# Optimization experiments

Hardware: AMD Instinct MI355X
Metric: run time of the kernel (lower is better)

Reference implementation:

```python
import jax, jax.numpy as jnp
import numpy as np

NEG_SLOPE = 0.01  # torch LeakyReLU default

def setup_inputs() -> dict:
    key = jax.random.key(0)
    ks = jax.random.split(key, 16)
    B, T = 256, 168
    LAG, LAT, WS, H = 168, 128, 64, 1024
    def lin(kw, kb, out_f, in_f):
        bound = 1.0 / np.sqrt(in_f)
        W = jax.random.uniform(kw, (out_f, in_f), jnp.float32, -bound, bound)
        b = jax.random.uniform(kb, (out_f,), jnp.float32, -bound, bound)
        return W, b
    W1, b1 = lin(ks[0], ks[1], 64, LAG)
    W2, b2 = lin(ks[2], ks[3], LAT, 64)
    W3, b3 = lin(ks[4], ks[5], H, LAT)
    bound = 1.0 / np.sqrt(H)
    Wih = jax.random.uniform(ks[6], (3 * H, WS), jnp.float32, -bound, bound)
    Whh = jax.random.uniform(ks[7], (3 * H, H), jnp.float32, -bound, bound)
    bih = jax.random.uniform(ks[8], (3 * H,), jnp.float32, -bound, bound)
    bhh = jax.random.uniform(ks[9], (3 * H,), jnp.float32, -bound, bound)
    Wo, bo = lin(ks[10], ks[11], 1, H)
    lag = jax.random.normal(ks[12], (B, LAG), jnp.float32)
    curr = jax.random.normal(ks[13], (T, B, WS), jnp.float32)
    return dict(lag=lag, curr=curr, W1=W1, b1=b1, W2=W2, b2=b2, W3=W3, b3=b3,
                Wih=Wih, Whh=Whh, bih=bih, bhh=bhh, Wo=Wo, bo=bo)

def _leaky(x):
    return jnp.where(x >= 0, x, NEG_SLOPE * x)

def reference(lag, curr, W1, b1, W2, b2, W3, b3, Wih, Whh, bih, bhh, Wo, bo):
    # Encoder MLP: lag -> 64 -> latent -> hidden (leaky relu after first two)
    h = _leaky(lag @ W1.T + b1)
    h = _leaky(h @ W2.T + b2)
    h0 = h @ W3.T + b3  # [B, H]
    H = h0.shape[-1]

    def step(h_t, x_t):
        gi = x_t @ Wih.T + bih          # [B, 3H]
        gh = h_t @ Whh.T + bhh          # [B, 3H]
        ir, iz, inn = jnp.split(gi, 3, axis=-1)
        hr, hz, hn = jnp.split(gh, 3, axis=-1)
        r = jax.nn.sigmoid(ir + hr)
        z = jax.nn.sigmoid(iz + hz)
        n = jnp.tanh(inn + r * hn)
        h_new = (1.0 - z) * n + z * h_t
        return h_new, h_new

    _, hs = jax.lax.scan(step, h0, curr)          # hs: [T, B, H]
    preds = jnp.squeeze(hs @ Wo.T + bo, -1)       # [T, B]
    return preds.T                                 # [B, T]
```

## Files before the change

### kernel.cpp

```cpp
#include <hip/hip_runtime.h>
#include <hip/hip_bf16.h>
#include <cstdint>
#include <cstddef>

typedef _Float16 half8 __attribute__((ext_vector_type(8)));
typedef _Float16 half4 __attribute__((ext_vector_type(4)));
typedef float floatx4 __attribute__((ext_vector_type(4)));
typedef unsigned long long u64;

#define B_ 256
#define T_ 168
#define H_ 1024
#define WS_ 64
#define LAG_ 168
#define LAT_ 128
#define SENT 0xFFFFFFFFFFFFFFFFull

__device__ __forceinline__ float fast_sigmoid(float x) {
    return __builtin_amdgcn_rcpf(1.f + __expf(-x));
}
__device__ __forceinline__ float fast_tanh(float x) {
    return 1.f - 2.f * __builtin_amdgcn_rcpf(__expf(2.f * x) + 1.f);
}

__global__ void cvt_all(const float4* __restrict__ a, half4* __restrict__ da, int na,
                        const float4* __restrict__ b, half4* __restrict__ db, int nb,
                        const float4* __restrict__ c, half4* __restrict__ dc, int nc) {
    int i = blockIdx.x * blockDim.x + threadIdx.x;
    const float4* s;
    half4* d;
    int j = i;
    if (j < na) { s = a; d = da; }
    else {
        j -= na;
        if (j < nb) { s = b; d = db; }
        else {
            j -= nb;
            if (j >= nc) return;
            s = c; d = dc;
        }
    }
    float4 v = s[j];
    half4 o;
    o[0] = (_Float16)v.x; o[1] = (_Float16)v.y;
    o[2] = (_Float16)v.z; o[3] = (_Float16)v.w;
    d[j] = o;
}

__global__ void enc_fused(const float* __restrict__ lag,
                          const float* __restrict__ W1, const float* __restrict__ b1,
                          const float* __restrict__ W2, const float* __restrict__ b2,
                          const float* __restrict__ W3, const float* __restrict__ b3,
                          float* __restrict__ hprev32, _Float16* __restrict__ h0f16) {
    __shared__ float lrow[LAG_];
    __shared__ float l1[64];
    __shared__ float l2[LAT_];
    const int r = blockIdx.x, tid = threadIdx.x;
    if (tid < LAG_) lrow[tid] = lag[(size_t)r * LAG_ + tid];
    __syncthreads();
    if (tid < 64) {
        const float* w = W1 + (size_t)tid * LAG_;
        float s = b1[tid];
        for (int k = 0; k < LAG_; ++k) s += lrow[k] * w[k];
        l1[tid] = (s >= 0.f) ? s : 0.01f * s;
    }
    __syncthreads();
    if (tid < LAT_) {
        const float* w = W2 + (size_t)tid * 64;
        float s = b2[tid];
        for (int k = 0; k < 64; ++k) s += l1[k] * w[k];
        l2[tid] = (s >= 0.f) ? s : 0.01f * s;
    }
    __syncthreads();
    for (int j = tid; j < H_; j += 256) {
        const float* w = W3 + (size_t)j * LAT_;
        float acc = b3[j];
        #pragma unroll 8
        for (int k = 0; k < LAT_; ++k) acc += l2[k] * w[k];
        hprev32[(size_t)r * H_ + j] = acc;
        h0f16[(size_t)r * H_ + j]   = (_Float16)acc;
    }
}

__global__ __launch_bounds__(256, 1) void gru_sentinel(
    _Float16* __restrict__ hring,
    const float* __restrict__ hprev32, const _Float16* __restrict__ whh16,
    const _Float16* __restrict__ wih16, const _Float16* __restrict__ x16,
    const float* __restrict__ bih, const float* __restrict__ bhh,
    const float* __restrict__ Wo, float* __restrict__ partials)
{
    __shared__ __align__(16) _Float16 Ash[2][16 * 1032];
    __shared__ __align__(16) _Float16 Wsh[192 * 72];
    __shared__ __align__(16) _Float16 Hsh[4 * 256];

    const int tid  = threadIdx.x;
    const int w    = tid >> 6;
    const int lane = tid & 63;
    const int m16  = lane & 15;
    const int quad = lane >> 4;
    const int pi   = blockIdx.x & 15;
    const int qi   = blockIdx.x >> 4;
    const int pi16 = pi << 4;
    const int u    = (qi << 6) + (w << 4) + m16;

    for (int idx = tid; idx < 1536; idx += 256) {
        int rowl = idx >> 3, ch = idx & 7;
        int g = rowl >> 6, ru = rowl & 63;
        *(uint4*)(&Wsh[rowl * 72 + (ch << 3)]) =
            *(const uint4*)(wih16 + (size_t)(((g << 10) + (qi << 6) + ru) << 6) + (ch << 3));
    }

    half8 br[32], bz[32], bn[32];
    {
        const _Float16* p0 = whh16 + ((size_t)u << 10) + (quad << 3);
        const _Float16* p1 = whh16 + ((size_t)(H_ + u) << 10) + (quad << 3);
        const _Float16* p2 = whh16 + ((size_t)(2 * H_ + u) << 10) + (quad << 3);
        #pragma unroll
        for (int c = 0; c < 32; ++c) br[c] = *(const half8*)(p0 + (c << 5));
        #pragma unroll
        for (int c = 0; c < 32; ++c) bz[c] = *(const half8*)(p1 + (c << 5));
        #pragma unroll
        for (int c = 0; c < 32; ++c) bn[c] = *(const half8*)(p2 + (c << 5));
    }

    const float b_r  = bih[u]          + bhh[u];
    const float b_z  = bih[H_ + u]     + bhh[H_ + u];
    const float b_in = bih[2 * H_ + u];
    const float b_hn = bhh[2 * H_ + u];
    const float wo_u = Wo[u];

    float hreg[4];
    #pragma unroll
    for (int i = 0; i < 4; ++i)
        hreg[i] = hprev32[((size_t)(pi16 + (quad << 2) + i) << 10) + u];

    __syncthreads();

    const int srow = tid >> 4;
    const int sch  = tid & 15;
    const int prow = lane >> 2;
    const int pc4  = lane & 3;

    for (int t = 0; t < T_; ++t) {
        const _Float16* hsrc = hring + (size_t)t * (B_ * H_);
        _Float16*       hdst = hring + (size_t)(t + 1) * (B_ * H_);

        half8 ax0 = *(const half8*)(x16 + (((size_t)t << 8) + pi16 + m16) * WS_ + (quad << 3));
        half8 ax1 = *(const half8*)(x16 + (((size_t)t << 8) + pi16 + m16) * WS_ + 32 + (quad << 3));

        u64 va[4][4];
        const _Float16* s = hsrc + ((size_t)(pi16 + srow) << 10) + (sch << 4);
        #pragma unroll
        for (int g = 0; g < 4; ++g)
            #pragma unroll
            for (int k = 0; k < 4; ++k)
                va[g][k] = __hip_atomic_load((const u64*)(s + (g << 8) + (k << 2)),
                                             __ATOMIC_RELAXED, __HIP_MEMORY_SCOPE_AGENT);

        floatx4 acc_r  = {b_r,  b_r,  b_r,  b_r };
        floatx4 acc_z  = {b_z,  b_z,  b_z,  b_z };
        floatx4 acc_in = {b_in, b_in, b_in, b_in};
        floatx4 acc_hn = {b_hn, b_hn, b_hn, b_hn};

        {
            half8 p0 = *(const half8*)(&Wsh[((w << 4) + m16) * 72        + (quad << 3)]);
            half8 p1 = *(const half8*)(&Wsh[(64 + (w << 4) + m16) * 72   + (quad << 3)]);
            half8 p2 = *(const half8*)(&Wsh[(128 + (w << 4) + m16) * 72  + (quad << 3)]);
            acc_r  = __builtin_amdgcn_mfma_f32_16x16x32_f16(ax0, p0, acc_r,  0, 0, 0);
            acc_z  = __builtin_amdgcn_mfma_f32_16x16x32_f16(ax0, p1, acc_z,  0, 0, 0);
            acc_in = __builtin_amdgcn_mfma_f32_16x16x32_f16(ax0, p2, acc_in, 0, 0, 0);
            half8 q0 = *(const half8*)(&Wsh[((w << 4) + m16) * 72        + 32 + (quad << 3)]);
            half8 q1 = *(const half8*)(&Wsh[(64 + (w << 4) + m16) * 72   + 32 + (quad << 3)]);
            half8 q2 = *(const half8*)(&Wsh[(128 + (w << 4) + m16) * 72  + 32 + (quad << 3)]);
            acc_r  = __builtin_amdgcn_mfma_f32_16x16x32_f16(ax1, q0, acc_r,  0, 0, 0);
            acc_z  = __builtin_amdgcn_mfma_f32_16x16x32_f16(ax1, q1, acc_z,  0, 0, 0);
            acc_in = __builtin_amdgcn_mfma_f32_16x16x32_f16(ax1, q2, acc_in, 0, 0, 0);
        }

        for (;;) {
            bool miss = false;
            #pragma unroll
            for (int g = 0; g < 4; ++g)
                #pragma unroll
                for (int k = 0; k < 4; ++k)
                    miss |= (va[g][k] == SENT);
            if (!__any(miss)) break;
            __builtin_amdgcn_s_sleep(1);
            #pragma unroll
            for (int g = 0; g < 4; ++g)
                #pragma unroll
                for (int k = 0; k < 4; ++k)
                    if (va[g][k] == SENT)
                        va[g][k] = __hip_atomic_load((const u64*)(s + (g << 8) + (k << 2)),
                                                     __ATOMIC_RELAXED, __HIP_MEMORY_SCOPE_AGENT);
        }

        {
            _Float16* dbase = &Ash[t & 1][srow * 1032 + (sch << 4)];
            #pragma unroll
            for (int g = 0; g < 4; ++g) {
                _Float16* d = dbase + (g << 8);
                *(u64*)(d + 0)  = va[g][0];
                *(u64*)(d + 4)  = va[g][1];
                *(u64*)(d + 8)  = va[g][2];
                *(u64*)(d + 12) = va[g][3];
            }
        }
        __syncthreads();

        const _Float16* abase = &Ash[t & 1][m16 * 1032 + (quad << 3)];
        #pragma unroll
        for (int c = 0; c < 32; ++c) {
            half8 a = *(const half8*)(abase + (c << 5));
            acc_r  = __builtin_amdgcn_mfma_f32_16x16x32_f16(a, br[c], acc_r,  0, 0, 0);
            acc_z  = __builtin_amdgcn_mfma_f32_16x16x32_f16(a, bz[c], acc_z,  0, 0, 0);
            acc_hn = __builtin_amdgcn_mfma_f32_16x16x32_f16(a, bn[c], acc_hn, 0, 0, 0);
        }

        float pv[4];
        #pragma unroll
        for (int i = 0; i < 4; ++i) {
            float rg = fast_sigmoid(acc_r[i]);
            float zg = fast_sigmoid(acc_z[i]);
            float ng = fast_tanh(acc_in[i] + rg * acc_hn[i]);
            float hn2 = (1.f - zg) * ng + zg * hreg[i];
            hreg[i] = hn2;
            pv[i] = hn2 * wo_u;
            Hsh[(w << 8) + ((quad << 2) + i) * 16 + m16] = (_Float16)hn2;
        }
        __threadfence_block();
        {
            u64 hv = *(const u64*)(&Hsh[(w << 8) + prow * 16 + (pc4 << 2)]);
            __hip_atomic_store(
                (u64*)(hdst + ((size_t)(pi16 + prow) << 10) + (qi << 6) + (w << 4) + (pc4 << 2)),
                hv, __ATOMIC_RELAXED, __HIP_MEMORY_SCOPE_AGENT);
        }

        #pragma unroll
        for (int m = 1; m < 16; m <<= 1) {
            #pragma unroll
            for (int i = 0; i < 4; ++i) pv[i] += __shfl_xor(pv[i], m);
        }
        if (m16 == 0) {
            #pragma unroll
            for (int i = 0; i < 4; ++i)
                partials[((size_t)(t << 6) + (qi << 2) + w) * 256 + pi16 + (quad << 2) + i] = pv[i];
        }
    }
}

__global__ __launch_bounds__(256, 1) void gru_flags(
    _Float16* __restrict__ hbuf,
    const float* __restrict__ hprev32, const _Float16* __restrict__ whh16,
    const _Float16* __restrict__ wih16, const _Float16* __restrict__ x16,
    const float* __restrict__ bih, const float* __restrict__ bhh,
    const float* __restrict__ Wo, float* __restrict__ partials,
    unsigned* __restrict__ bar)
{
    __shared__ __align__(16) _Float16 Ash[16 * 1032];
    __shared__ __align__(16) _Float16 Wsh[192 * 72];
    __shared__ __align__(16) _Float16 Hsh[4 * 256];

    const int tid  = threadIdx.x;
    const int w    = tid >> 6;
    const int lane = tid & 63;
    const int m16  = lane & 15;
    const int quad = lane >> 4;
    const int pi   = blockIdx.x & 15;
    const int qi   = blockIdx.x >> 4;
    const int pi16 = pi << 4;
    const int u    = (qi << 6) + (w << 4) + m16;

    for (int idx = tid; idx < 1536; idx += 256) {
        int rowl = idx >> 3, ch = idx & 7;
        int g = rowl >> 6, ru = rowl & 63;
        *(uint4*)(&Wsh[rowl * 72 + (ch << 3)]) =
            *(const uint4*)(wih16 + (size_t)(((g << 10) + (qi << 6) + ru) << 6) + (ch << 3));
    }

    half8 br[32], bz[32];
    {
        const _Float16* p0 = whh16 + ((size_t)u << 10) + (quad << 3);
        const _Float16* p1 = whh16 + ((size_t)(H_ + u) << 10) + (quad << 3);
        #pragma unroll
        for (int c = 0; c < 32; ++c) br[c] = *(const half8*)(p0 + (c << 5));
        #pragma unroll
        for (int c = 0; c < 32; ++c) bz[c] = *(const half8*)(p1 + (c << 5));
    }
    const _Float16* bnp = whh16 + ((size_t)(2 * H_ + u) << 10) + (quad << 3);

    const float b_r  = bih[u]          + bhh[u];
    const float b_z  = bih[H_ + u]     + bhh[H_ + u];
    const float b_in = bih[2 * H_ + u];
    const float b_hn = bhh[2 * H_ + u];
    const float wo_u = Wo[u];

    float hreg[4];
    #pragma unroll
    for (int i = 0; i < 4; ++i)
        hreg[i] = hprev32[((size_t)(pi16 + (quad << 2) + i) << 10) + u];

    __syncthreads();

    unsigned* flag_self       = bar + (((pi << 4) | qi) << 4);
    const unsigned* flag_peer = bar + (((pi << 4) | (lane & 15)) << 4);
    const int srow = tid >> 4;
    const int sch  = tid & 15;
    const int prow = lane >> 2;
    const int pc4  = lane & 3;

    for (int t = 0; t < T_; ++t) {
        const _Float16* hsrc = hbuf + (size_t)(t & 3) * (B_ * H_);
        _Float16*       hdst = hbuf + (size_t)((t + 1) & 3) * (B_ * H_);

        half8 ax0 = *(const half8*)(x16 + (((size_t)t << 8) + pi16 + m16) * WS_ + (quad << 3));
        half8 ax1 = *(const half8*)(x16 + (((size_t)t << 8) + pi16 + m16) * WS_ + 32 + (quad << 3));
        half8 bnA[8], bnB[8];
        #pragma unroll
        for (int j = 0; j < 8; ++j) bnA[j] = *(const half8*)(bnp + (j << 5));

        const unsigned need = (unsigned)t;
        u64 rdy = 0;

        while ((rdy & 0xFull) != 0xFull) {
            unsigned f = 0;
            if (lane < 16)
                f = __hip_atomic_load(flag_peer, __ATOMIC_RELAXED, __HIP_MEMORY_SCOPE_AGENT);
            rdy |= __ballot(f >= need);
            if ((rdy & 0xFull) != 0xFull) __builtin_amdgcn_s_sleep(1);
        }
        u64 va0, va1, va2, va3;
        {
            const _Float16* s = hsrc + ((size_t)(pi16 + srow) << 10) + (sch << 4);
            va0 = __hip_atomic_load((const u64*)(s + 0),  __ATOMIC_RELAXED, __HIP_MEMORY_SCOPE_AGENT);
            va1 = __hip_atomic_load((const u64*)(s + 4),  __ATOMIC_RELAXED, __HIP_MEMORY_SCOPE_AGENT);
            va2 = __hip_atomic_load((const u64*)(s + 8),  __ATOMIC_RELAXED, __HIP_MEMORY_SCOPE_AGENT);
            va3 = __hip_atomic_load((const u64*)(s + 12), __ATOMIC_RELAXED, __HIP_MEMORY_SCOPE_AGENT);
        }

        floatx4 acc_r  = {b_r,  b_r,  b_r,  b_r };
        floatx4 acc_z  = {b_z,  b_z,  b_z,  b_z };
        floatx4 acc_in = {b_in, b_in, b_in, b_in};
        floatx4 acc_hn = {b_hn, b_hn, b_hn, b_hn};

        {
            half8 p0 = *(const half8*)(&Wsh[((w << 4) + m16) * 72        + (quad << 3)]);
            half8 p1 = *(const half8*)(&Wsh[(64 + (w << 4) + m16) * 72   + (quad << 3)]);
            half8 p2 = *(const half8*)(&Wsh[(128 + (w << 4) + m16) * 72  + (quad << 3)]);
            acc_r  = __builtin_amdgcn_mfma_f32_16x16x32_f16(ax0, p0, acc_r,  0, 0, 0);
            acc_z  = __builtin_amdgcn_mfma_f32_16x16x32_f16(ax0, p1, acc_z,  0, 0, 0);
            acc_in = __builtin_amdgcn_mfma_f32_16x16x32_f16(ax0, p2, acc_in, 0, 0, 0);
            half8 q0 = *(const half8*)(&Wsh[((w << 4) + m16) * 72        + 32 + (quad << 3)]);
            half8 q1 = *(const half8*)(&Wsh[(64 + (w << 4) + m16) * 72   + 32 + (quad << 3)]);
            half8 q2 = *(const half8*)(&Wsh[(128 + (w << 4) + m16) * 72  + 32 + (quad << 3)]);
            acc_r  = __builtin_amdgcn_mfma_f32_16x16x32_f16(ax1, q0, acc_r,  0, 0, 0);
            acc_z  = __builtin_amdgcn_mfma_f32_16x16x32_f16(ax1, q1, acc_z,  0, 0, 0);
            acc_in = __builtin_amdgcn_mfma_f32_16x16x32_f16(ax1, q2, acc_in, 0, 0, 0);
        }

        #pragma unroll
        for (int g = 0; g < 4; ++g) {
            {
                _Float16* d = &Ash[srow * 1032 + (g << 8) + (sch << 4)];
                *(u64*)(d + 0)  = va0;
                *(u64*)(d + 4)  = va1;
                *(u64*)(d + 8)  = va2;
                *(u64*)(d + 12) = va3;
            }
            __syncthreads();
            if (g < 3) {
                const u64 mask = 0xFull << ((g + 1) << 2);
                while ((rdy & mask) != mask) {
                    unsigned f = 0;
                    if (lane < 16)
                        f = __hip_atomic_load(flag_peer, __ATOMIC_RELAXED, __HIP_MEMORY_SCOPE_AGENT);
                    rdy |= __ballot(f >= need);
                    if ((rdy & mask) != mask) __builtin_amdgcn_s_sleep(1);
                }
                const _Float16* s = hsrc + ((size_t)(pi16 + srow) << 10) + ((g + 1) << 8) + (sch << 4);
                va0 = __hip_atomic_load((const u64*)(s + 0),  __ATOMIC_RELAXED, __HIP_MEMORY_SCOPE_AGENT);
                va1 = __hip_atomic_load((const u64*)(s + 4),  __ATOMIC_RELAXED, __HIP_MEMORY_SCOPE_AGENT);
                va2 = __hip_atomic_load((const u64*)(s + 8),  __ATOMIC_RELAXED, __HIP_MEMORY_SCOPE_AGENT);
                va3 = __hip_atomic_load((const u64*)(s + 12), __ATOMIC_RELAXED, __HIP_MEMORY_SCOPE_AGENT);
                #pragma unroll
                for (int j = 0; j < 8; ++j)
                    bnB[j] = *(const half8*)(bnp + ((((g + 1) << 3) + j) << 5));
            }
            #pragma unroll
            for (int j = 0; j < 8; ++j) {
                const int c = (g << 3) + j;
                half8 a = *(const half8*)(&Ash[m16 * 1032 + (c << 5) + (quad << 3)]);
                acc_r  = __builtin_amdgcn_mfma_f32_16x16x32_f16(a, br[c], acc_r,  0, 0, 0);
                acc_z  = __builtin_amdgcn_mfma_f32_16x16x32_f16(a, bz[c], acc_z,  0, 0, 0);
                acc_hn = __builtin_amdgcn_mfma_f32_16x16x32_f16(a, bnA[j], acc_hn, 0, 0, 0);
            }
            if (g < 3) {
                #pragma unroll
                for (int j = 0; j < 8; ++j) bnA[j] = bnB[j];
            }
        }

        float pv[4];
        #pragma unroll
        for (int i = 0; i < 4; ++i) {
            float rg = fast_sigmoid(acc_r[i]);
            float zg = fast_sigmoid(acc_z[i]);
            float ng = fast_tanh(acc_in[i] + rg * acc_hn[i]);
            float hn2 = (1.f - zg) * ng + zg * hreg[i];
            hreg[i] = hn2;
            pv[i] = hn2 * wo_u;
            Hsh[(w << 8) + ((quad << 2) + i) * 16 + m16] = (_Float16)hn2;
        }
        __threadfence_block();
        {
            u64 hv = *(const u64*)(&Hsh[(w << 8) + prow * 16 + (pc4 << 2)]);
            __hip_atomic_store(
                (u64*)(hdst + ((size_t)(pi16 + prow) << 10) + (qi << 6) + (w << 4) + (pc4 << 2)),
                hv, __ATOMIC_RELAXED, __HIP_MEMORY_SCOPE_AGENT);
        }
        #pragma unroll
        for (int m = 1; m < 16; m <<= 1) {
            #pragma unroll
            for (int i = 0; i < 4; ++i) pv[i] += __shfl_xor(pv[i], m);
        }
        asm volatile("s_waitcnt vmcnt(0)" ::: "memory");
        __syncthreads();
        if (tid == 0)
            __hip_atomic_store(flag_self, (unsigned)(t + 1),
                               __ATOMIC_RELAXED, __HIP_MEMORY_SCOPE_AGENT);
        if (m16 == 0) {
            #pragma unroll
            for (int i = 0; i < 4; ++i)
                partials[((size_t)(t << 6) + (qi << 2) + w) * 256 + pi16 + (quad << 2) + i] = pv[i];
        }
    }
}

__global__ void out_reduce(const float* __restrict__ partials, const float* __restrict__ bo,
                           float* __restrict__ out) {
    int t = blockIdx.x, r = threadIdx.x;
    float s = 0.f;
    #pragma unroll
    for (int k = 0; k < 64; ++k) s += partials[((size_t)(t << 6) + k) * 256 + r];
    out[(size_t)r * T_ + t] = s + bo[0];
}

extern "C" void kernel_launch(void* const* d_in, const int* in_sizes, int n_in,
                              void* d_out, int out_size, void* d_ws, size_t ws_size,
                              hipStream_t stream) {
    const float* lag  = (const float*)d_in[0];
    const float* curr = (const float*)d_in[1];
    const float* W1   = (const float*)d_in[2];
    const float* b1   = (const float*)d_in[3];
    const float* W2   = (const float*)d_in[4];
    const float* b2   = (const float*)d_in[5];
    const float* W3   = (const float*)d_in[6];
    const float* b3   = (const float*)d_in[7];
    const float* Wih  = (const float*)d_in[8];
    const float* Whh  = (const float*)d_in[9];
    const float* bih  = (const float*)d_in[10];
    const float* bhh  = (const float*)d_in[11];
    const float* Wo   = (const float*)d_in[12];
    const float* bo   = (const float*)d_in[13];
    float* out = (float*)d_out;

    char* ws = (char*)d_ws;
    size_t off = 0;
    auto alloc = [&](size_t bytes) -> void* {
        void* p = ws + off;
        off += (bytes + 255) & ~(size_t)255;
        return p;
    };
    _Float16* whh16 = (_Float16*)alloc((size_t)3 * H_ * H_ * 2);
    _Float16* wih16 = (_Float16*)alloc((size_t)3 * H_ * WS_ * 2);
    _Float16* x16   = (_Float16*)alloc((size_t)T_ * B_ * WS_ * 2);
    float* hprev32  = (float*)alloc((size_t)B_ * H_ * 4);
    float* partials = (float*)alloc((size_t)T_ * B_ * 64 * 4);
    unsigned* bar   = (unsigned*)alloc(81920);

    const size_t slot_bytes = (size_t)B_ * H_ * 2;
    const size_t ring_bytes = (size_t)(T_ + 1) * slot_bytes;
    const bool sentinel_mode = (ws_size >= off + ring_bytes + 4096);
    _Float16* hring = (_Float16*)alloc(sentinel_mode ? ring_bytes : 4 * slot_bytes);

    if (sentinel_mode) {
        hipMemsetAsync((char*)hring + slot_bytes, 0xFF, ring_bytes - slot_bytes, stream);
    } else {
        hipMemsetAsync(bar, 0, 81920, stream);
    }

    const int na = 3 * H_ * H_ / 4;
    const int nb = 3 * H_ * WS_ / 4;
    const int nc = T_ * B_ * WS_ / 4;
    const int ntot = na + nb + nc;
    cvt_all<<<(ntot + 255) / 256, 256, 0, stream>>>(
        (const float4*)Whh, (half4*)whh16, na,
        (const float4*)Wih, (half4*)wih16, nb,
        (const float4*)curr, (half4*)x16, nc);

    enc_fused<<<B_, 256, 0, stream>>>(lag, W1, b1, W2, b2, W3, b3, hprev32, hring);

    if (sentinel_mode)
        gru_sentinel<<<dim3(256), dim3(256), 0, stream>>>(
            hring, hprev32, whh16, wih16, x16, bih, bhh, Wo, partials);
    else
        gru_flags<<<dim3(256), dim3(256), 0, stream>>>(
            hring, hprev32, whh16, wih16, x16, bih, bhh, Wo, partials, bar);

    out_reduce<<<T_, B_, 0, stream>>>(partials, bo, out);
}
```

Measured before the change: 953.1 us.

## Chunk hidden-state wait into four K-slices and stream Whh n-gate weights

The persistent GRU kernel no longer keeps the n-gate Whh slice in registers. Each step reloads it from global memory in 8-chunk pieces, double-buffered, which frees a third of the weight registers. The spin-wait on the previous hidden state is split into four K-chunks, so MFMA work on chunk g can start while later chunks are still arriving. The cost is four block barriers per step instead of one, plus extra global or L2 traffic for the n-gate weights every step.

```diff
diff --git a/kernel.cpp b/kernel.cpp
--- a/kernel.cpp
+++ b/kernel.cpp
@@ -110,18 +110,16 @@
             *(const uint4*)(wih16 + (size_t)(((g << 10) + (qi << 6) + ru) << 6) + (ch << 3));
     }
 
-    half8 br[32], bz[32], bn[32];
+    half8 br[32], bz[32];
     {
         const _Float16* p0 = whh16 + ((size_t)u << 10) + (quad << 3);
         const _Float16* p1 = whh16 + ((size_t)(H_ + u) << 10) + (quad << 3);
-        const _Float16* p2 = whh16 + ((size_t)(2 * H_ + u) << 10) + (quad << 3);
         #pragma unroll
         for (int c = 0; c < 32; ++c) br[c] = *(const half8*)(p0 + (c << 5));
         #pragma unroll
         for (int c = 0; c < 32; ++c) bz[c] = *(const half8*)(p1 + (c << 5));
-        #pragma unroll
-        for (int c = 0; c < 32; ++c) bn[c] = *(const half8*)(p2 + (c << 5));
-    }
+    }
+    const _Float16* bnp = whh16 + ((size_t)(2 * H_ + u) << 10) + (quad << 3);
 
     const float b_r  = bih[u]          + bhh[u];
     const float b_z  = bih[H_ + u]     + bhh[H_ + u];
@@ -147,15 +145,17 @@
 
         half8 ax0 = *(const half8*)(x16 + (((size_t)t << 8) + pi16 + m16) * WS_ + (quad << 3));
         half8 ax1 = *(const half8*)(x16 + (((size_t)t << 8) + pi16 + m16) * WS_ + 32 + (quad << 3));
-
-        u64 va[4][4];
-        const _Float16* s = hsrc + ((size_t)(pi16 + srow) << 10) + (sch << 4);
-        #pragma unroll
-        for (int g = 0; g < 4; ++g)
-            #pragma unroll
-            for (int k = 0; k < 4; ++k)
-                va[g][k] = __hip_atomic_load((const u64*)(s + (g << 8) + (k << 2)),
-                                             __ATOMIC_RELAXED, __HIP_MEMORY_SCOPE_AGENT);
+        half8 bnA[8], bnB[8];
+        #pragma unroll
+        for (int j = 0; j < 8; ++j) bnA[j] = *(const half8*)(bnp + (j << 5));
+
+        const _Float16* sbase = hsrc + ((size_t)(pi16 + srow) << 10) + (sch << 4);
+
+        u64 va0, va1, va2, va3;
+        va0 = __hip_atomic_load((const u64*)(sbase + 0),  __ATOMIC_RELAXED, __HIP_MEMORY_SCOPE_AGENT);
+        va1 = __hip_atomic_load((const u64*)(sbase + 4),  __ATOMIC_RELAXED, __HIP_MEMORY_SCOPE_AGENT);
+        va2 = __hip_atomic_load((const u64*)(sbase + 8),  __ATOMIC_RELAXED, __HIP_MEMORY_SCOPE_AGENT);
+        va3 = __hip_atomic_load((const u64*)(sbase + 12), __ATOMIC_RELAXED, __HIP_MEMORY_SCOPE_AGENT);
 
         floatx4 acc_r  = {b_r,  b_r,  b_r,  b_r };
         floatx4 acc_z  = {b_z,  b_z,  b_z,  b_z };
@@ -177,44 +177,48 @@
             acc_in = __builtin_amdgcn_mfma_f32_16x16x32_f16(ax1, q2, acc_in, 0, 0, 0);
         }
 
-        for (;;) {
-            bool miss = false;
+        #pragma unroll
+        for (int g = 0; g < 4; ++g) {
+            for (;;) {
+                bool miss = (va0 == SENT) | (va1 == SENT) | (va2 == SENT) | (va3 == SENT);
+                if (!__any(miss)) break;
+                __builtin_amdgcn_s_sleep(1);
+                const _Float16* sp = sbase + (g << 8);
+                if (va0 == SENT) va0 = __hip_atomic_load((const u64*)(sp + 0),  __ATOMIC_RELAXED, __HIP_MEMORY_SCOPE_AGENT);
+                if (va1 == SENT) va1 = __hip_atomic_load((const u64*)(sp + 4),  __ATOMIC_RELAXED, __HIP_MEMORY_SCOPE_AGENT);
+                if (va2 == SENT) va2 = __hip_atomic_load((const u64*)(sp + 8),  __ATOMIC_RELAXED, __HIP_MEMORY_SCOPE_AGENT);
+                if (va3 == SENT) va3 = __hip_atomic_load((const u64*)(sp + 12), __ATOMIC_RELAXED, __HIP_MEMORY_SCOPE_AGENT);
+            }
+            {
+                _Float16* d = &Ash[t & 1][srow * 1032 + (g << 8) + (sch << 4)];
+                *(u64*)(d + 0)  = va0;
+                *(u64*)(d + 4)  = va1;
+                *(u64*)(d + 8)  = va2;
+                *(u64*)(d + 12) = va3;
+            }
+            __syncthreads();
+            if (g < 3) {
+                const _Float16* sn = sbase + ((g + 1) << 8);
+                va0 = __hip_atomic_load((const u64*)(sn + 0),  __ATOMIC_RELAXED, __HIP_MEMORY_SCOPE_AGENT);
+                va1 = __hip_atomic_load((const u64*)(sn + 4),  __ATOMIC_RELAXED, __HIP_MEMORY_SCOPE_AGENT);
+                va2 = __hip_atomic_load((const u64*)(sn + 8),  __ATOMIC_RELAXED, __HIP_MEMORY_SCOPE_AGENT);
+                va3 = __hip_atomic_load((const u64*)(sn + 12), __ATOMIC_RELAXED, __HIP_MEMORY_SCOPE_AGENT);
+                #pragma unroll
+                for (int j = 0; j < 8; ++j)
+                    bnB[j] = *(const half8*)(bnp + ((((g + 1) << 3) + j) << 5));
+            }
             #pragma unroll
-            for (int g = 0; g < 4; ++g)
+            for (int j = 0; j < 8; ++j) {
+                const int c = (g << 3) + j;
+                half8 a = *(const half8*)(&Ash[t & 1][m16 * 1032 + (c << 5) + (quad << 3)]);
+                acc_r  = __builtin_amdgcn_mfma_f32_16x16x32_f16(a, br[c], acc_r,  0, 0, 0);
+                acc_z  = __builtin_amdgcn_mfma_f32_16x16x32_f16(a, bz[c], acc_z,  0, 0, 0);
+                acc_hn = __builtin_amdgcn_mfma_f32_16x16x32_f16(a, bnA[j], acc_hn, 0, 0, 0);
+            }
+            if (g < 3) {
                 #pragma unroll
-                for (int k = 0; k < 4; ++k)
-                    miss |= (va[g][k] == SENT);
-            if (!__any(miss)) break;
-            __builtin_amdgcn_s_sleep(1);
-            #pragma unroll
-            for (int g = 0; g < 4; ++g)
-                #pragma unroll
-                for (int k = 0; k < 4; ++k)
-                    if (va[g][k] == SENT)
-                        va[g][k] = __hip_atomic_load((const u64*)(s + (g << 8) + (k << 2)),
-                                                     __ATOMIC_RELAXED, __HIP_MEMORY_SCOPE_AGENT);
-        }
-
-        {
-            _Float16* dbase = &Ash[t & 1][srow * 1032 + (sch << 4)];
-            #pragma unroll
-            for (int g = 0; g < 4; ++g) {
-                _Float16* d = dbase + (g << 8);
-                *(u64*)(d + 0)  = va[g][0];
-                *(u64*)(d + 4)  = va[g][1];
-                *(u64*)(d + 8)  = va[g][2];
-                *(u64*)(d + 12) = va[g][3];
-            }
-        }
-        __syncthreads();
-
-        const _Float16* abase = &Ash[t & 1][m16 * 1032 + (quad << 3)];
-        #pragma unroll
-        for (int c = 0; c < 32; ++c) {
-            half8 a = *(const half8*)(abase + (c << 5));
-            acc_r  = __builtin_amdgcn_mfma_f32_16x16x32_f16(a, br[c], acc_r,  0, 0, 0);
-            acc_z  = __builtin_amdgcn_mfma_f32_16x16x32_f16(a, bz[c], acc_z,  0, 0, 0);
-            acc_hn = __builtin_amdgcn_mfma_f32_16x16x32_f16(a, bn[c], acc_hn, 0, 0, 0);
+                for (int j = 0; j < 8; ++j) bnA[j] = bnB[j];
+            }
         }
 
         float pv[4];
@@ -235,7 +239,6 @@
                 (u64*)(hdst + ((size_t)(pi16 + prow) << 10) + (qi << 6) + (w << 4) + (pc4 << 2)),
                 hv, __ATOMIC_RELAXED, __HIP_MEMORY_SCOPE_AGENT);
         }
-
         #pragma unroll
         for (int m = 1; m < 16; m <<= 1) {
             #pragma unroll
```

After: 1.182 ms. 1.24x slower.
